# Optimization experiments

Measured on AMD Instinct MI355X. Metric: run time of the kernel, lower is better.

## Reference

```python
import jax, jax.numpy as jnp
import numpy as np

# GATConv hyperparams hardcoded in InterGraphAttention: out_channels=32, heads=2
H = 2
C = 32
N_H = 50000
N_T = 50000
E = 1600000
D = 128
NEG_SLOPE = 0.2


def setup_inputs() -> dict:
    key = jax.random.key(0)
    ks = jax.random.split(key, 9)
    h_x = jax.random.normal(ks[0], (N_H, D), dtype=jnp.float32)
    t_x = jax.random.normal(ks[1], (N_T, D), dtype=jnp.float32)
    src = jax.random.randint(ks[2], (E,), 0, N_H)
    dst = jax.random.randint(ks[3], (E,), 0, N_T)
    # PyG's add_self_loops path first removes existing self-loops; generate edges without any
    dst = jnp.where(dst == src, (dst + 1) % N_T, dst)
    edge_index = jnp.stack([src, dst]).astype(jnp.int64)
    glorot = 1.0 / np.sqrt(D)
    W_src = jax.random.normal(ks[4], (D, H * C), dtype=jnp.float32) * glorot
    W_dst = jax.random.normal(ks[5], (D, H * C), dtype=jnp.float32) * glorot
    att_src = jax.random.normal(ks[6], (H, C), dtype=jnp.float32) * (1.0 / np.sqrt(C))
    att_dst = jax.random.normal(ks[7], (H, C), dtype=jnp.float32) * (1.0 / np.sqrt(C))
    bias = jnp.zeros((H * C,), dtype=jnp.float32)
    return {"h_x": h_x, "t_x": t_x, "edge_index": edge_index,
            "W_src": W_src, "W_dst": W_dst,
            "att_src": att_src, "att_dst": att_dst, "bias": bias}


def _gat(x_src, x_dst, src, dst, W_s, W_d, a_src, a_dst, bias):
    Ns, Nd = x_src.shape[0], x_dst.shape[0]
    xs = (x_src @ W_s).reshape(Ns, H, C)   # [Ns,H,C]
    xd = (x_dst @ W_d).reshape(Nd, H, C)   # [Nd,H,C]
    al_s = jnp.einsum('nhc,hc->nh', xs, a_src)  # [Ns,H]
    al_d = jnp.einsum('nhc,hc->nh', xd, a_dst)  # [Nd,H]
    # PyG GATConv default add_self_loops=True: append i->i for i < min(Ns,Nd)
    loop = jnp.arange(min(Ns, Nd), dtype=src.dtype)
    src2 = jnp.concatenate([src, loop])
    dst2 = jnp.concatenate([dst, loop])
    alpha = jax.nn.leaky_relu(al_s[src2] + al_d[dst2], NEG_SLOPE)  # [E2,H]
    # edge-softmax over destination neighborhoods (PyG softmax: +1e-16 in denom)
    m = jax.ops.segment_max(alpha, dst2, num_segments=Nd)
    e = jnp.exp(alpha - m[dst2])
    s = jax.ops.segment_sum(e, dst2, num_segments=Nd)
    w = e / (s[dst2] + 1e-16)                                      # [E2,H]
    msg = w[:, :, None] * xs[src2]                                 # [E2,H,C]
    out = jax.ops.segment_sum(msg, dst2, num_segments=Nd)          # [Nd,H,C]
    return out.reshape(Nd, H * C) + bias


def reference(h_x, t_x, edge_index, W_src, W_dst, att_src, att_dst, bias):
    h_in = jax.nn.elu(h_x)
    t_in = jax.nn.elu(t_x)
    src, dst = edge_index[0], edge_index[1]
    t_rep = _gat(h_in, t_in, src, dst, W_src, W_dst, att_src, att_dst, bias)
    h_rep = _gat(t_in, h_in, dst, src, W_src, W_dst, att_src, att_dst, bias)
    return (h_rep, t_rep)
```

## Files before the change

### kernel.cpp

```cpp
#include <hip/hip_runtime.h>
#include <hip/hip_bf16.h>
#include <math.h>

#define HC 64
#define DD 128
#define BSH 7
#define BW  128
#define KMAX 512
#define CHUNK 4096
#define CAP 8192
#define CAPB 6144

typedef __attribute__((ext_vector_type(8))) short bf16x8;
typedef __attribute__((ext_vector_type(4))) float f32x4;

__device__ __forceinline__ unsigned short f2bf(float f) {
  unsigned u = __float_as_uint(f);
  return (unsigned short)((u + 0x7fffu + ((u >> 16) & 1u)) >> 16);
}

__global__ __launch_bounds__(128) void build_bt(
    const float* __restrict__ Wsrc, const float* __restrict__ Wdst,
    const float* __restrict__ att_src, const float* __restrict__ att_dst,
    unsigned short* __restrict__ Bt, int* __restrict__ gcur, int KK)
{
  int j = blockIdx.x;
  int k = threadIdx.x;
  const float LOG2E = 1.44269504f;
  float v = 0.f;
  if (j < 64) {
    v = Wsrc[k * HC + j];
  } else if (j < 68) {
    int hh = j - 64;
    const float* W = (hh < 2) ? Wsrc : Wdst;
    const float* a = (hh < 2) ? att_src : att_dst;
    int h = hh & 1;
    float s = 0.f;
    for (int c = 0; c < 32; ++c)
      s = fmaf(W[k * HC + h * 32 + c], a[h * 32 + c], s);
    v = s * LOG2E;
  }
  Bt[j * DD + k] = f2bf(v);
  if (j == 0) {
    for (int i = k; i < KK; i += 128) gcur[i] = 0;
  }
}

__global__ __launch_bounds__(512) void fused_front(
    const float* __restrict__ xH, const float* __restrict__ xT,
    const unsigned short* __restrict__ Bt,
    __hip_bfloat16* __restrict__ xsH, __hip_bfloat16* __restrict__ xsT,
    float* __restrict__ lsH, float* __restrict__ ldH,
    float* __restrict__ lsT, float* __restrict__ ldT,
    int NH, int NT, int blocksH, int nodeB,
    const int* __restrict__ src, const int* __restrict__ dst, int E, int NL,
    int* __restrict__ gcurA, int* __restrict__ gcurB,
    unsigned int* __restrict__ partA, unsigned int* __restrict__ partB,
    int KA, int KB)
{
  __shared__ unsigned int raw[CHUNK];
  __shared__ unsigned int stage[CHUNK];
  __shared__ int lcnt[KMAX];
  __shared__ int lbase[KMAX];
  __shared__ int lcur[KMAX];
  __shared__ int gbase[KMAX];

  int tid = threadIdx.x;

  if ((int)blockIdx.x < nodeB) {
    const float* x; __hip_bfloat16* xs; float* logit_s; float* logit_d; int N, blk;
    if ((int)blockIdx.x < blocksH) { x = xH; xs = xsH; logit_s = lsH; logit_d = ldH; N = NH; blk = blockIdx.x; }
    else { x = xT; xs = xsT; logit_s = lsT; logit_d = ldT; N = NT; blk = blockIdx.x - blocksH; }

    int wid  = tid >> 6;
    int lane = tid & 63;
    int m    = lane & 15;
    int kg   = lane >> 4;
    int nbase = (blk * 8 + wid) * 16;
    if (nbase >= N) return;
    int nrow = nbase + m;
    int nclamp = (nrow < N) ? nrow : (N - 1);

    bf16x8 ahi[4], alo[4];
    const float* xrow = x + (size_t)nclamp * DD + kg * 8;
    #pragma unroll
    for (int kt = 0; kt < 4; ++kt) {
      float4 v0 = *(const float4*)(xrow + kt * 32);
      float4 v1 = *(const float4*)(xrow + kt * 32 + 4);
      float vv[8] = {v0.x, v0.y, v0.z, v0.w, v1.x, v1.y, v1.z, v1.w};
      #pragma unroll
      for (int i = 0; i < 8; ++i) {
        float v = vv[i];
        v = (v > 0.f) ? v : (exp2f(v * 1.44269504f) - 1.f);
        unsigned hb = __float_as_uint(v) & 0xffff0000u;
        ahi[kt][i] = (short)(hb >> 16);
        alo[kt][i] = (short)f2bf(v - __uint_as_float(hb));
      }
    }

    f32x4 acc[5];
    #pragma unroll
    for (int ct = 0; ct < 5; ++ct) acc[ct] = (f32x4){0.f, 0.f, 0.f, 0.f};
    const unsigned short* bbase = Bt + m * DD + kg * 8;
    #pragma unroll
    for (int ct = 0; ct < 5; ++ct) {
      #pragma unroll
      for (int kt = 0; kt < 4; ++kt) {
        bf16x8 b = *(const bf16x8*)(bbase + ct * 16 * DD + kt * 32);
        acc[ct] = __builtin_amdgcn_mfma_f32_16x16x32_bf16(ahi[kt], b, acc[ct], 0, 0, 0);
        acc[ct] = __builtin_amdgcn_mfma_f32_16x16x32_bf16(alo[kt], b, acc[ct], 0, 0, 0);
      }
    }

    int r0 = kg * 4;
    unsigned short* xsu = (unsigned short*)xs;
    #pragma unroll
    for (int ct = 0; ct < 4; ++ct) {
      #pragma unroll
      for (int r = 0; r < 4; ++r) {
        int n = nbase + r0 + r;
        if (n < N) xsu[(size_t)n * HC + ct * 16 + m] = f2bf(acc[ct][r]);
      }
    }
    if (m < 4) {
      float* dstp = (m < 2) ? logit_s : logit_d;
      int h = m & 1;
      #pragma unroll
      for (int r = 0; r < 4; ++r) {
        int n = nbase + r0 + r;
        if (n < N) dstp[n * 2 + h] = acc[4][r];
      }
    }
    return;
  }

  int bid = blockIdx.x - nodeB;
  int base = bid * CHUNK;
  int E2 = E + NL;
  int lim = base + CHUNK < E2 ? base + CHUNK : E2;
  int cnt = lim - base;

  for (int i = base + tid; i < lim; i += 512) {
    unsigned s, d;
    if (i < E) { s = (unsigned)src[i]; d = (unsigned)dst[i]; }
    else       { s = d = (unsigned)(i - E); }
    raw[i - base] = s | (d << 16);
  }
  __syncthreads();

  for (int p = 0; p < 2; ++p) {
    const int K = p ? KB : KA;
    int* gcur = p ? gcurB : gcurA;
    unsigned int* outp = p ? partB : partA;

    for (int k2 = tid; k2 < K; k2 += 512) lcnt[k2] = 0;
    __syncthreads();
    for (int i = tid; i < cnt; i += 512) {
      unsigned w = raw[i];
      unsigned key = p ? (w & 0xffffu) : (w >> 16);
      atomicAdd(&lcnt[key >> BSH], 1);
    }
    __syncthreads();
    if (tid < 64) {
      int carry = 0;
      for (int c0 = 0; c0 < K; c0 += 64) {
        int c = c0 + tid;
        int v = (c < K) ? lcnt[c] : 0;
        int inc = v;
        #pragma unroll
        for (int o = 1; o < 64; o <<= 1) {
          int u = __shfl_up(inc, o, 64);
          if (tid >= o) inc += u;
        }
        if (c < K) lbase[c] = inc - v + carry;
        carry += __shfl(inc, 63, 64);
      }
    }
    __syncthreads();
    for (int k2 = tid; k2 < K; k2 += 512) {
      lcur[k2] = lbase[k2];
      gbase[k2] = atomicAdd(&gcur[k2], lcnt[k2]);
    }
    __syncthreads();
    for (int i = tid; i < cnt; i += 512) {
      unsigned w = raw[i];
      unsigned key = p ? (w & 0xffffu) : (w >> 16);
      unsigned val = p ? (w >> 16) : (w & 0xffffu);
      int pos = atomicAdd(&lcur[key >> BSH], 1);
      stage[pos] = val | (key << 16);
    }
    __syncthreads();
    for (int i = tid; i < cnt; i += 512) {
      unsigned wv = stage[i];
      int kk = wv >> (16 + BSH);
      outp[(size_t)kk * CAPB + gbase[kk] + (i - lbase[kk])] = wv;
    }
    __syncthreads();
  }
}

__global__ __launch_bounds__(256) void bucket_csr4(
    const unsigned int* __restrict__ partA, const int* __restrict__ cntA,
    int KA, int NA,
    const unsigned int* __restrict__ partB, const int* __restrict__ cntB,
    int KB, int NB,
    int E2, int* __restrict__ csrA, int* __restrict__ rowA,
    int* __restrict__ csrB, int* __restrict__ rowB)
{
  __shared__ int sbuf[CAP];
  __shared__ int hist[BW + 1];
  __shared__ int cur[BW];
  __shared__ int red[256];
  const unsigned int* part; const int* cntp;
  int* csr; int* row; int k, K, N;
  if ((int)blockIdx.x < KA) { k = blockIdx.x; part = partA; cntp = cntA; csr = csrA; row = rowA; K = KA; N = NA; }
  else { k = blockIdx.x - KA; part = partB; cntp = cntB; csr = csrB; row = rowB; K = KB; N = NB; }
  int tid = threadIdx.x;

  int psum = 0;
  for (int j = tid; j < k; j += 256) psum += cntp[j];
  red[tid] = psum; __syncthreads();
  for (int s = 128; s > 0; s >>= 1) {
    if (tid < s) red[tid] += red[tid + s];
    __syncthreads();
  }
  int beg = red[0];
  int cnt = cntp[k];
  size_t kbase = (size_t)k * CAPB;
  int d0 = k << BSH;
  int width = (BW < N - d0) ? BW : (N - d0);

  for (int i = tid; i <= BW; i += 256) hist[i] = 0;
  __syncthreads();
  for (int i = tid; i < cnt; i += 256)
    atomicAdd(&hist[(part[kbase + i] >> 16) & (BW - 1)], 1);
  __syncthreads();
  if (tid == 0) {
    int run = 0;
    for (int j = 0; j < width; ++j) { int c = hist[j]; hist[j] = run; run += c; }
    hist[width] = run;
  }
  __syncthreads();
  if (tid < width) { cur[tid] = hist[tid]; row[d0 + tid] = beg + hist[tid]; }
  if (k == K - 1 && tid == 0) row[N] = E2;
  __syncthreads();
  if (cnt <= CAP) {
    for (int i = tid; i < cnt; i += 256) {
      unsigned int wv = part[kbase + i];
      int pos = atomicAdd(&cur[(wv >> 16) & (BW - 1)], 1);
      sbuf[pos] = wv & 0xFFFF;
    }
    __syncthreads();
    for (int i = tid; i < cnt; i += 256) csr[beg + i] = sbuf[i];
  } else {
    for (int i = tid; i < cnt; i += 256) {
      unsigned int wv = part[kbase + i];
      int pos = atomicAdd(&cur[(wv >> 16) & (BW - 1)], 1);
      csr[beg + pos] = wv & 0xFFFF;
    }
  }
}

__device__ __forceinline__ float lrelu_clamp(float a) {
  a = (a > 0.f) ? a : 0.2f * a;
  return fminf(a, 43.f);
}

__global__ __launch_bounds__(256) void csr_message5(
    const int* __restrict__ rowA, const int* __restrict__ csrA,
    const float* __restrict__ lsA, const float* __restrict__ ldA,
    const __hip_bfloat16* __restrict__ xsA, float* __restrict__ outA, int NdA,
    const int* __restrict__ rowB, const int* __restrict__ csrB,
    const float* __restrict__ lsB, const float* __restrict__ ldB,
    const __hip_bfloat16* __restrict__ xsB, float* __restrict__ outB, int NdB,
    const float* __restrict__ bias, int blocksA)
{
  const int* row; const int* csr_src; const float* logit_s; const float* logit_d;
  const __hip_bfloat16* xs; float* out; int Nd, blk;
  if ((int)blockIdx.x < blocksA) { row = rowA; csr_src = csrA; logit_s = lsA; logit_d = ldA; xs = xsA; out = outA; Nd = NdA; blk = blockIdx.x; }
  else { row = rowB; csr_src = csrB; logit_s = lsB; logit_d = ldB; xs = xsB; out = outB; Nd = NdB; blk = blockIdx.x - blocksA; }

  __shared__ int lds[4 * 232];
  int tid  = threadIdx.x;
  int wid  = tid >> 6;
  int lane = tid & 63;
  int l31  = lane & 31;
  int half = lane >> 5;
  int head = l31 >> 4;

  int* L = &lds[wid * 232];
  float* Lf = (float*)L;
  int sv_w = (half ? 40 : 0) + l31;
  int w0_w = (half ? 160 : 80) + l31;
  int w1_w = (half ? 200 : 120) + l31;
  const int4*   svq = (const int4*)  (L  + (half ? 40 : 0));
  const float4* wq  = (const float4*)(Lf + (half ? (head ? 200 : 160)
                                                 : (head ? 120 : 80)));
  const unsigned* xs2 = (const unsigned*)xs;
  const float2* ls2 = (const float2*)logit_s;

  int d = blk * 8 + (wid << 1) + half;
  int beg = 0, end = 0;
  float2 ld2 = {0.f, 0.f};
  if (d < Nd) {
    beg = row[d]; end = row[d + 1];
    ld2 = ((const float2*)logit_d)[d];
  }

  int nt = ((end - beg) + 31) >> 5;
  nt = max(nt, __shfl_xor(nt, 32, 64));

  float2 accA = {0.f, 0.f}, accB = {0.f, 0.f};
  float s0 = 0.f, s1 = 0.f;
  int myPos = beg;

#define STEP(SV, W, ACC) {                                         \
    unsigned xv = xs2[(SV) * 32 + l31];                            \
    ACC.x = fmaf((W), __uint_as_float(xv << 16), ACC.x);           \
    ACC.y = fmaf((W), __uint_as_float(xv & 0xffff0000u), ACC.y);   \
  }

  for (int tile = 0; tile < nt; ++tile, myPos += 32) {
    int tc = end - myPos; tc = tc < 0 ? 0 : (tc > 32 ? 32 : tc);
    int sv = 0; float e0 = 0.f, e1 = 0.f;
    if (l31 < tc) {
      sv = csr_src[myPos + l31];
      float2 l2 = ls2[sv];
      e0 = exp2f(lrelu_clamp(l2.x + ld2.x));
      e1 = exp2f(lrelu_clamp(l2.y + ld2.y));
    }
    s0 += e0; s1 += e1;
    L[sv_w]       = sv;
    Lf[w0_w]      = e0;
    Lf[w1_w]      = e1;
    asm volatile("s_waitcnt lgkmcnt(0)" ::: "memory");
    int tcmax = max(tc, __shfl_xor(tc, 32, 64));
    int nq = (tcmax + 3) >> 2;
    for (int q = 0; q < nq; ++q) {
      int4   s4 = svq[q];
      float4 w4 = wq[q];
      STEP(s4.x, w4.x, accA)
      STEP(s4.y, w4.y, accB)
      STEP(s4.z, w4.z, accA)
      STEP(s4.w, w4.w, accB)
    }
  }
#undef STEP

  #pragma unroll
  for (int off = 16; off > 0; off >>= 1) {
    s0 += __shfl_xor(s0, off, 64);
    s1 += __shfl_xor(s1, off, 64);
  }
  float sD = (l31 & 16) ? s1 : s0;
  float inv = 1.f / (sD + 1e-16f);

  if (d < Nd) {
    float2 b2 = ((const float2*)bias)[l31];
    float2 o;
    o.x = (accA.x + accB.x) * inv + b2.x;
    o.y = (accA.y + accB.y) * inv + b2.y;
    ((float2*)out)[(size_t)d * 32 + l31] = o;
  }
}

extern "C" void kernel_launch(void* const* d_in, const int* in_sizes, int n_in,
                              void* d_out, int out_size, void* d_ws, size_t ws_size,
                              hipStream_t stream)
{
  const float* h_x   = (const float*)d_in[0];
  const float* t_x   = (const float*)d_in[1];
  const int*   edge  = (const int*)d_in[2];
  const float* W_src = (const float*)d_in[3];
  const float* W_dst = (const float*)d_in[4];
  const float* att_s = (const float*)d_in[5];
  const float* att_d = (const float*)d_in[6];
  const float* bias  = (const float*)d_in[7];

  int NH = in_sizes[0] / DD;
  int NT = in_sizes[1] / DD;
  int E  = in_sizes[2] / 2;
  int NL = (NH < NT) ? NH : NT;
  int E2 = E + NL;
  const int* srcA = edge;
  const int* dstA = edge + E;

  int KA = (NT + BW - 1) >> BSH;
  int KB = (NH + BW - 1) >> BSH;
  int B  = (E2 + CHUNK - 1) / CHUNK;

  char* w = (char*)d_ws;
  size_t used = 0;
  auto alloc = [&](size_t bytes) {
    char* p = w + used; used = (used + bytes + 255) & ~(size_t)255; return p;
  };
  __hip_bfloat16* xsA = (__hip_bfloat16*)alloc((size_t)NH * HC * 2);
  __hip_bfloat16* xsB = (__hip_bfloat16*)alloc((size_t)NT * HC * 2);
  float* lsA  = (float*)alloc((size_t)NH * 2 * 4);
  float* ldB  = (float*)alloc((size_t)NH * 2 * 4);
  float* lsB  = (float*)alloc((size_t)NT * 2 * 4);
  float* ldA  = (float*)alloc((size_t)NT * 2 * 4);
  int* gcur   = (int*)alloc((size_t)(KA + KB) * 4);
  int* gcurA  = gcur;
  int* gcurB  = gcur + KA;
  int* rowT   = (int*)alloc((size_t)(NT + 1) * 4);
  int* rowH   = (int*)alloc((size_t)(NH + 1) * 4);
  unsigned int* partA = (unsigned int*)alloc((size_t)KA * CAPB * 4);
  unsigned int* partB = (unsigned int*)alloc((size_t)KB * CAPB * 4);
  int* csrT   = (int*)alloc((size_t)E2 * 4);
  int* csrH   = (int*)alloc((size_t)E2 * 4);
  unsigned short* Bt = (unsigned short*)alloc((size_t)80 * DD * 2);

  float* out   = (float*)d_out;
  float* out_h = out;
  float* out_t = out + (size_t)NH * HC;

  build_bt<<<80, 128, 0, stream>>>(W_src, W_dst, att_s, att_d, Bt,
                                   gcur, KA + KB);

  int bH = (NH + 127) / 128, bT = (NT + 127) / 128;
  int nodeB = bH + bT;
  fused_front<<<nodeB + B, 512, 0, stream>>>(
      h_x, t_x, Bt, xsA, xsB, lsA, ldB, lsB, ldA, NH, NT, bH, nodeB,
      srcA, dstA, E, NL, gcurA, gcurB, partA, partB, KA, KB);

  bucket_csr4<<<KA + KB, 256, 0, stream>>>(
      partA, gcurA, KA, NT, partB, gcurB, KB, NH,
      E2, csrT, rowT, csrH, rowH);

  int gA = (NT + 7) / 8, gB = (NH + 7) / 8;
  csr_message5<<<gA + gB, 256, 0, stream>>>(
      rowT, csrT, lsA, ldA, xsA, out_t, NT,
      rowH, csrH, lsB, ldB, xsB, out_h, NH, bias, gA);
}
```

Before: 221.3 us.

## Fuse all stages into one persistent cooperative kernel with grid syncs

Replaces the four separate launches (weight prep, projection plus edge partitioning, bucket-to-CSR, message aggregation) with a single persistent cooperative kernel. Stages are separated by grid.sync, and each block loops over tiles, chunks, buckets and node groups. The goal is to remove launch gaps and inter-kernel drain and fill. In exchange, the grid size is capped by occupancy, weight prep runs on a single block, LDS use grows to the union of all stages, and message blocks change shape from 256 to 512 threads. The old multi-kernel path is kept as a fallback when cooperative launch is unavailable.

```diff
diff --git a/kernel.cpp b/kernel.cpp
--- a/kernel.cpp
+++ b/kernel.cpp
@@ -1,6 +1,9 @@
 #include <hip/hip_runtime.h>
 #include <hip/hip_bf16.h>
+#include <hip/hip_cooperative_groups.h>
 #include <math.h>
+
+namespace cg = cooperative_groups;
 
 #define HC 64
 #define DD 128
@@ -17,6 +20,329 @@
 __device__ __forceinline__ unsigned short f2bf(float f) {
   unsigned u = __float_as_uint(f);
   return (unsigned short)((u + 0x7fffu + ((u >> 16) & 1u)) >> 16);
+}
+
+__device__ __forceinline__ float lrelu_clamp(float a) {
+  a = (a > 0.f) ? a : 0.2f * a;
+  return fminf(a, 43.f);
+}
+
+struct MegaArgs {
+  const float* h_x; const float* t_x;
+  const float* Wsrc; const float* Wdst;
+  const float* att_src; const float* att_dst;
+  const float* bias;
+  const int* src; const int* dst;
+  unsigned short* Bt;
+  __hip_bfloat16* xsA; __hip_bfloat16* xsB;
+  float* lsA; float* ldB; float* lsB; float* ldA;
+  int* gcurA; int* gcurB;
+  int* rowT; int* rowH;
+  unsigned* partA; unsigned* partB;
+  int* csrT; int* csrH;
+  float* out_h; float* out_t;
+  int NH, NT, E, NL, KA, KB;
+};
+
+union SMem {
+  struct { unsigned raw[CHUNK]; unsigned stage[CHUNK];
+           int lcnt[KMAX]; int lbase[KMAX]; int lcur[KMAX]; int gbase[KMAX]; } part;
+  struct { int sbuf[CAP]; int hist[BW + 1]; int cur[BW]; int red[512]; } bkt;
+  struct { int lds[8 * 232]; } msg;
+};
+
+__global__ __launch_bounds__(512) void mega(MegaArgs a)
+{
+  cg::grid_group grid = cg::this_grid();
+  __shared__ SMem sm;
+  const int tid = threadIdx.x;
+  const int E2 = a.E + a.NL;
+  const int tilesH = (a.NH + 127) >> 7, tilesT = (a.NT + 127) >> 7;
+  const int ntiles = tilesH + tilesT;
+  const int nchunks = (E2 + CHUNK - 1) / CHUNK;
+  const float LOG2E = 1.44269504f;
+
+  if (blockIdx.x == 0) {
+    for (int i = tid; i < 80 * DD; i += 512) {
+      int j = i >> 7, k = i & 127;
+      float v = 0.f;
+      if (j < 64) {
+        v = a.Wsrc[k * HC + j];
+      } else if (j < 68) {
+        int hh = j - 64;
+        const float* W = (hh < 2) ? a.Wsrc : a.Wdst;
+        const float* at = (hh < 2) ? a.att_src : a.att_dst;
+        int h = hh & 1;
+        float s = 0.f;
+        for (int c = 0; c < 32; ++c)
+          s = fmaf(W[k * HC + h * 32 + c], at[h * 32 + c], s);
+        v = s * LOG2E;
+      }
+      a.Bt[j * DD + k] = f2bf(v);
+    }
+  } else if (blockIdx.x == 1) {
+    for (int i = tid; i < a.KA + a.KB; i += 512) a.gcurA[i] = 0;
+  }
+  __threadfence();
+  grid.sync();
+
+  for (int it = blockIdx.x; it < ntiles + nchunks; it += gridDim.x) {
+    if (it < ntiles) {
+      const float* x; __hip_bfloat16* xs; float* logit_s; float* logit_d; int N, blk;
+      if (it < tilesH) { x = a.h_x; xs = a.xsA; logit_s = a.lsA; logit_d = a.ldB; N = a.NH; blk = it; }
+      else { x = a.t_x; xs = a.xsB; logit_s = a.lsB; logit_d = a.ldA; N = a.NT; blk = it - tilesH; }
+      int wid = tid >> 6, lane = tid & 63, m = lane & 15, kg = lane >> 4;
+      int nbase = (blk * 8 + wid) * 16;
+      if (nbase < N) {
+        int nrow = nbase + m;
+        int nclamp = (nrow < N) ? nrow : (N - 1);
+        bf16x8 ahi[4], alo[4];
+        const float* xrow = x + (size_t)nclamp * DD + kg * 8;
+        #pragma unroll
+        for (int kt = 0; kt < 4; ++kt) {
+          float4 v0 = *(const float4*)(xrow + kt * 32);
+          float4 v1 = *(const float4*)(xrow + kt * 32 + 4);
+          float vv[8] = {v0.x, v0.y, v0.z, v0.w, v1.x, v1.y, v1.z, v1.w};
+          #pragma unroll
+          for (int i = 0; i < 8; ++i) {
+            float v = vv[i];
+            v = (v > 0.f) ? v : (exp2f(v * 1.44269504f) - 1.f);
+            unsigned hb = __float_as_uint(v) & 0xffff0000u;
+            ahi[kt][i] = (short)(hb >> 16);
+            alo[kt][i] = (short)f2bf(v - __uint_as_float(hb));
+          }
+        }
+        f32x4 acc[5];
+        #pragma unroll
+        for (int ct = 0; ct < 5; ++ct) acc[ct] = (f32x4){0.f, 0.f, 0.f, 0.f};
+        const unsigned short* bbase = a.Bt + m * DD + kg * 8;
+        #pragma unroll
+        for (int ct = 0; ct < 5; ++ct) {
+          #pragma unroll
+          for (int kt = 0; kt < 4; ++kt) {
+            bf16x8 b = *(const bf16x8*)(bbase + ct * 16 * DD + kt * 32);
+            acc[ct] = __builtin_amdgcn_mfma_f32_16x16x32_bf16(ahi[kt], b, acc[ct], 0, 0, 0);
+            acc[ct] = __builtin_amdgcn_mfma_f32_16x16x32_bf16(alo[kt], b, acc[ct], 0, 0, 0);
+          }
+        }
+        int r0 = kg * 4;
+        unsigned short* xsu = (unsigned short*)xs;
+        #pragma unroll
+        for (int ct = 0; ct < 4; ++ct) {
+          #pragma unroll
+          for (int r = 0; r < 4; ++r) {
+            int n = nbase + r0 + r;
+            if (n < N) xsu[(size_t)n * HC + ct * 16 + m] = f2bf(acc[ct][r]);
+          }
+        }
+        if (m < 4) {
+          float* dstp = (m < 2) ? logit_s : logit_d;
+          int h = m & 1;
+          #pragma unroll
+          for (int r = 0; r < 4; ++r) {
+            int n = nbase + r0 + r;
+            if (n < N) dstp[n * 2 + h] = acc[4][r];
+          }
+        }
+      }
+    } else {
+      int bid = it - ntiles;
+      int base = bid * CHUNK;
+      int lim = base + CHUNK < E2 ? base + CHUNK : E2;
+      int cnt = lim - base;
+      for (int i = base + tid; i < lim; i += 512) {
+        unsigned s, d;
+        if (i < a.E) { s = (unsigned)a.src[i]; d = (unsigned)a.dst[i]; }
+        else         { s = d = (unsigned)(i - a.E); }
+        sm.part.raw[i - base] = s | (d << 16);
+      }
+      __syncthreads();
+      for (int p = 0; p < 2; ++p) {
+        const int K = p ? a.KB : a.KA;
+        int* gcur = p ? a.gcurB : a.gcurA;
+        unsigned* outp = p ? a.partB : a.partA;
+        for (int k2 = tid; k2 < K; k2 += 512) sm.part.lcnt[k2] = 0;
+        __syncthreads();
+        for (int i = tid; i < cnt; i += 512) {
+          unsigned w = sm.part.raw[i];
+          unsigned key = p ? (w & 0xffffu) : (w >> 16);
+          atomicAdd(&sm.part.lcnt[key >> BSH], 1);
+        }
+        __syncthreads();
+        if (tid < 64) {
+          int carry = 0;
+          for (int c0 = 0; c0 < K; c0 += 64) {
+            int c = c0 + tid;
+            int v = (c < K) ? sm.part.lcnt[c] : 0;
+            int inc = v;
+            #pragma unroll
+            for (int o = 1; o < 64; o <<= 1) {
+              int u = __shfl_up(inc, o, 64);
+              if (tid >= o) inc += u;
+            }
+            if (c < K) sm.part.lbase[c] = inc - v + carry;
+            carry += __shfl(inc, 63, 64);
+          }
+        }
+        __syncthreads();
+        for (int k2 = tid; k2 < K; k2 += 512) {
+          sm.part.lcur[k2] = sm.part.lbase[k2];
+          sm.part.gbase[k2] = atomicAdd(&gcur[k2], sm.part.lcnt[k2]);
+        }
+        __syncthreads();
+        for (int i = tid; i < cnt; i += 512) {
+          unsigned w = sm.part.raw[i];
+          unsigned key = p ? (w & 0xffffu) : (w >> 16);
+          unsigned val = p ? (w >> 16) : (w & 0xffffu);
+          int pos = atomicAdd(&sm.part.lcur[key >> BSH], 1);
+          sm.part.stage[pos] = val | (key << 16);
+        }
+        __syncthreads();
+        for (int i = tid; i < cnt; i += 512) {
+          unsigned wv = sm.part.stage[i];
+          int kk = wv >> (16 + BSH);
+          outp[(size_t)kk * CAPB + sm.part.gbase[kk] + (i - sm.part.lbase[kk])] = wv;
+        }
+        __syncthreads();
+      }
+    }
+  }
+  __threadfence();
+  grid.sync();
+
+  for (int bb = blockIdx.x; bb < a.KA + a.KB; bb += gridDim.x) {
+    const unsigned* part; const int* cntp; int* csr; int* row; int k, K, N;
+    if (bb < a.KA) { k = bb; part = a.partA; cntp = a.gcurA; csr = a.csrT; row = a.rowT; K = a.KA; N = a.NT; }
+    else { k = bb - a.KA; part = a.partB; cntp = a.gcurB; csr = a.csrH; row = a.rowH; K = a.KB; N = a.NH; }
+
+    int psum = 0;
+    for (int j = tid; j < k; j += 512) psum += cntp[j];
+    sm.bkt.red[tid] = psum; __syncthreads();
+    for (int s = 256; s > 0; s >>= 1) {
+      if (tid < s) sm.bkt.red[tid] += sm.bkt.red[tid + s];
+      __syncthreads();
+    }
+    int beg = sm.bkt.red[0];
+    int cnt = cntp[k];
+    size_t kbase = (size_t)k * CAPB;
+    int d0 = k << BSH;
+    int width = (BW < N - d0) ? BW : (N - d0);
+
+    for (int i = tid; i <= BW; i += 512) sm.bkt.hist[i] = 0;
+    __syncthreads();
+    for (int i = tid; i < cnt; i += 512)
+      atomicAdd(&sm.bkt.hist[(part[kbase + i] >> 16) & (BW - 1)], 1);
+    __syncthreads();
+    if (tid == 0) {
+      int run = 0;
+      for (int j = 0; j < width; ++j) { int c = sm.bkt.hist[j]; sm.bkt.hist[j] = run; run += c; }
+      sm.bkt.hist[width] = run;
+    }
+    __syncthreads();
+    if (tid < width) { sm.bkt.cur[tid] = sm.bkt.hist[tid]; row[d0 + tid] = beg + sm.bkt.hist[tid]; }
+    if (k == K - 1 && tid == 0) row[N] = E2;
+    __syncthreads();
+    if (cnt <= CAP) {
+      for (int i = tid; i < cnt; i += 512) {
+        unsigned wv = part[kbase + i];
+        int pos = atomicAdd(&sm.bkt.cur[(wv >> 16) & (BW - 1)], 1);
+        sm.bkt.sbuf[pos] = wv & 0xFFFF;
+      }
+      __syncthreads();
+      for (int i = tid; i < cnt; i += 512) csr[beg + i] = sm.bkt.sbuf[i];
+    } else {
+      for (int i = tid; i < cnt; i += 512) {
+        unsigned wv = part[kbase + i];
+        int pos = atomicAdd(&sm.bkt.cur[(wv >> 16) & (BW - 1)], 1);
+        csr[beg + pos] = wv & 0xFFFF;
+      }
+    }
+    __syncthreads();
+  }
+  __threadfence();
+  grid.sync();
+
+  {
+    int wid = tid >> 6, lane = tid & 63, l31 = lane & 31, half = lane >> 5;
+    int head = l31 >> 4;
+    int* L = sm.msg.lds + wid * 232;
+    float* Lf = (float*)L;
+    int sv_w = (half ? 40 : 0) + l31;
+    int w0_w = (half ? 160 : 80) + l31;
+    int w1_w = (half ? 200 : 120) + l31;
+    const int4*   svq = (const int4*)  (L  + (half ? 40 : 0));
+    const float4* wq  = (const float4*)(Lf + (half ? (head ? 200 : 160)
+                                                   : (head ? 120 : 80)));
+    int ngA = (a.NT + 15) >> 4, ngB = (a.NH + 15) >> 4;
+    for (int g = blockIdx.x; g < ngA + ngB; g += gridDim.x) {
+      const int* row; const int* csr_src; const float* logit_s; const float* logit_d;
+      const __hip_bfloat16* xs; float* out; int Nd, gblk;
+      if (g < ngA) { row = a.rowT; csr_src = a.csrT; logit_s = a.lsA; logit_d = a.ldA; xs = a.xsA; out = a.out_t; Nd = a.NT; gblk = g; }
+      else { row = a.rowH; csr_src = a.csrH; logit_s = a.lsB; logit_d = a.ldB; xs = a.xsB; out = a.out_h; Nd = a.NH; gblk = g - ngA; }
+      const unsigned* xs2 = (const unsigned*)xs;
+      const float2* ls2 = (const float2*)logit_s;
+
+      int d = gblk * 16 + (wid << 1) + half;
+      int beg = 0, end = 0;
+      float2 ld2 = {0.f, 0.f};
+      if (d < Nd) {
+        beg = row[d]; end = row[d + 1];
+        ld2 = ((const float2*)logit_d)[d];
+      }
+      int nt = ((end - beg) + 31) >> 5;
+      nt = max(nt, __shfl_xor(nt, 32, 64));
+
+      float2 accA = {0.f, 0.f}, accB = {0.f, 0.f};
+      float s0 = 0.f, s1 = 0.f;
+      int myPos = beg;
+
+#define STEP(SV, W, ACC) {                                         \
+      unsigned xv = xs2[(SV) * 32 + l31];                          \
+      ACC.x = fmaf((W), __uint_as_float(xv << 16), ACC.x);         \
+      ACC.y = fmaf((W), __uint_as_float(xv & 0xffff0000u), ACC.y); \
+    }
+      for (int tile = 0; tile < nt; ++tile, myPos += 32) {
+        int tc = end - myPos; tc = tc < 0 ? 0 : (tc > 32 ? 32 : tc);
+        int sv = 0; float e0 = 0.f, e1 = 0.f;
+        if (l31 < tc) {
+          sv = csr_src[myPos + l31];
+          float2 l2 = ls2[sv];
+          e0 = exp2f(lrelu_clamp(l2.x + ld2.x));
+          e1 = exp2f(lrelu_clamp(l2.y + ld2.y));
+        }
+        s0 += e0; s1 += e1;
+        L[sv_w]  = sv;
+        Lf[w0_w] = e0;
+        Lf[w1_w] = e1;
+        asm volatile("s_waitcnt lgkmcnt(0)" ::: "memory");
+        int tcmax = max(tc, __shfl_xor(tc, 32, 64));
+        int nq = (tcmax + 3) >> 2;
+        for (int q = 0; q < nq; ++q) {
+          int4   s4 = svq[q];
+          float4 w4 = wq[q];
+          STEP(s4.x, w4.x, accA)
+          STEP(s4.y, w4.y, accB)
+          STEP(s4.z, w4.z, accA)
+          STEP(s4.w, w4.w, accB)
+        }
+      }
+#undef STEP
+      #pragma unroll
+      for (int off = 16; off > 0; off >>= 1) {
+        s0 += __shfl_xor(s0, off, 64);
+        s1 += __shfl_xor(s1, off, 64);
+      }
+      float sD = (l31 & 16) ? s1 : s0;
+      float inv = 1.f / (sD + 1e-16f);
+      if (d < Nd) {
+        float2 b2 = ((const float2*)a.bias)[l31];
+        float2 o;
+        o.x = (accA.x + accB.x) * inv + b2.x;
+        o.y = (accA.y + accB.y) * inv + b2.y;
+        ((float2*)out)[(size_t)d * 32 + l31] = o;
+      }
+    }
+  }
 }
 
 __global__ __launch_bounds__(128) void build_bt(
@@ -64,14 +390,12 @@
   __shared__ int lbase[KMAX];
   __shared__ int lcur[KMAX];
   __shared__ int gbase[KMAX];
-
   int tid = threadIdx.x;
 
   if ((int)blockIdx.x < nodeB) {
     const float* x; __hip_bfloat16* xs; float* logit_s; float* logit_d; int N, blk;
     if ((int)blockIdx.x < blocksH) { x = xH; xs = xsH; logit_s = lsH; logit_d = ldH; N = NH; blk = blockIdx.x; }
     else { x = xT; xs = xsT; logit_s = lsT; logit_d = ldT; N = NT; blk = blockIdx.x - blocksH; }
-
     int wid  = tid >> 6;
     int lane = tid & 63;
     int m    = lane & 15;
@@ -80,7 +404,6 @@
     if (nbase >= N) return;
     int nrow = nbase + m;
     int nclamp = (nrow < N) ? nrow : (N - 1);
-
     bf16x8 ahi[4], alo[4];
     const float* xrow = x + (size_t)nclamp * DD + kg * 8;
     #pragma unroll
@@ -97,7 +420,6 @@
         alo[kt][i] = (short)f2bf(v - __uint_as_float(hb));
       }
     }
-
     f32x4 acc[5];
     #pragma unroll
     for (int ct = 0; ct < 5; ++ct) acc[ct] = (f32x4){0.f, 0.f, 0.f, 0.f};
@@ -111,7 +433,6 @@
         acc[ct] = __builtin_amdgcn_mfma_f32_16x16x32_bf16(alo[kt], b, acc[ct], 0, 0, 0);
       }
     }
-
     int r0 = kg * 4;
     unsigned short* xsu = (unsigned short*)xs;
     #pragma unroll
@@ -139,7 +460,6 @@
   int E2 = E + NL;
   int lim = base + CHUNK < E2 ? base + CHUNK : E2;
   int cnt = lim - base;
-
   for (int i = base + tid; i < lim; i += 512) {
     unsigned s, d;
     if (i < E) { s = (unsigned)src[i]; d = (unsigned)dst[i]; }
@@ -147,12 +467,10 @@
     raw[i - base] = s | (d << 16);
   }
   __syncthreads();
-
   for (int p = 0; p < 2; ++p) {
     const int K = p ? KB : KA;
     int* gcur = p ? gcurB : gcurA;
     unsigned int* outp = p ? partB : partA;
-
     for (int k2 = tid; k2 < K; k2 += 512) lcnt[k2] = 0;
     __syncthreads();
     for (int i = tid; i < cnt; i += 512) {
@@ -216,7 +534,6 @@
   if ((int)blockIdx.x < KA) { k = blockIdx.x; part = partA; cntp = cntA; csr = csrA; row = rowA; K = KA; N = NA; }
   else { k = blockIdx.x - KA; part = partB; cntp = cntB; csr = csrB; row = rowB; K = KB; N = NB; }
   int tid = threadIdx.x;
-
   int psum = 0;
   for (int j = tid; j < k; j += 256) psum += cntp[j];
   red[tid] = psum; __syncthreads();
@@ -229,7 +546,6 @@
   size_t kbase = (size_t)k * CAPB;
   int d0 = k << BSH;
   int width = (BW < N - d0) ? BW : (N - d0);
-
   for (int i = tid; i <= BW; i += 256) hist[i] = 0;
   __syncthreads();
   for (int i = tid; i < cnt; i += 256)
@@ -259,11 +575,6 @@
       csr[beg + pos] = wv & 0xFFFF;
     }
   }
-}
-
-__device__ __forceinline__ float lrelu_clamp(float a) {
-  a = (a > 0.f) ? a : 0.2f * a;
-  return fminf(a, 43.f);
 }
 
 __global__ __launch_bounds__(256) void csr_message5(
@@ -279,7 +590,6 @@
   const __hip_bfloat16* xs; float* out; int Nd, blk;
   if ((int)blockIdx.x < blocksA) { row = rowA; csr_src = csrA; logit_s = lsA; logit_d = ldA; xs = xsA; out = outA; Nd = NdA; blk = blockIdx.x; }
   else { row = rowB; csr_src = csrB; logit_s = lsB; logit_d = ldB; xs = xsB; out = outB; Nd = NdB; blk = blockIdx.x - blocksA; }
-
   __shared__ int lds[4 * 232];
   int tid  = threadIdx.x;
   int wid  = tid >> 6;
@@ -287,7 +597,6 @@
   int l31  = lane & 31;
   int half = lane >> 5;
   int head = l31 >> 4;
-
   int* L = &lds[wid * 232];
   float* Lf = (float*)L;
   int sv_w = (half ? 40 : 0) + l31;
@@ -298,7 +607,6 @@
                                                  : (head ? 120 : 80)));
   const unsigned* xs2 = (const unsigned*)xs;
   const float2* ls2 = (const float2*)logit_s;
-
   int d = blk * 8 + (wid << 1) + half;
   int beg = 0, end = 0;
   float2 ld2 = {0.f, 0.f};
@@ -306,20 +614,16 @@
     beg = row[d]; end = row[d + 1];
     ld2 = ((const float2*)logit_d)[d];
   }
-
   int nt = ((end - beg) + 31) >> 5;
   nt = max(nt, __shfl_xor(nt, 32, 64));
-
   float2 accA = {0.f, 0.f}, accB = {0.f, 0.f};
   float s0 = 0.f, s1 = 0.f;
   int myPos = beg;
-
 #define STEP(SV, W, ACC) {                                         \
     unsigned xv = xs2[(SV) * 32 + l31];                            \
     ACC.x = fmaf((W), __uint_as_float(xv << 16), ACC.x);           \
     ACC.y = fmaf((W), __uint_as_float(xv & 0xffff0000u), ACC.y);   \
   }
-
   for (int tile = 0; tile < nt; ++tile, myPos += 32) {
     int tc = end - myPos; tc = tc < 0 ? 0 : (tc > 32 ? 32 : tc);
     int sv = 0; float e0 = 0.f, e1 = 0.f;
@@ -330,9 +634,9 @@
       e1 = exp2f(lrelu_clamp(l2.y + ld2.y));
     }
     s0 += e0; s1 += e1;
-    L[sv_w]       = sv;
-    Lf[w0_w]      = e0;
-    Lf[w1_w]      = e1;
+    L[sv_w]  = sv;
+    Lf[w0_w] = e0;
+    Lf[w1_w] = e1;
     asm volatile("s_waitcnt lgkmcnt(0)" ::: "memory");
     int tcmax = max(tc, __shfl_xor(tc, 32, 64));
     int nq = (tcmax + 3) >> 2;
@@ -346,7 +650,6 @@
     }
   }
 #undef STEP
-
   #pragma unroll
   for (int off = 16; off > 0; off >>= 1) {
     s0 += __shfl_xor(s0, off, 64);
@@ -354,7 +657,6 @@
   }
   float sD = (l31 & 16) ? s1 : s0;
   float inv = 1.f / (sD + 1e-16f);
-
   if (d < Nd) {
     float2 b2 = ((const float2*)bias)[l31];
     float2 o;
@@ -415,19 +717,52 @@
   float* out_h = out;
   float* out_t = out + (size_t)NH * HC;
 
+  static int coop = -1;
+  static int gridSize = 0;
+  if (coop < 0) {
+    int dev = 0; hipGetDevice(&dev);
+    int ca = 0;
+    hipDeviceGetAttribute(&ca, hipDeviceAttributeCooperativeLaunch, dev);
+    int nCU = 0;
+    hipDeviceGetAttribute(&nCU, hipDeviceAttributeMultiprocessorCount, dev);
+    int nbpc = 0;
+    hipError_t e = hipOccupancyMaxActiveBlocksPerMultiprocessor(
+        &nbpc, (const void*)mega, 512, 0);
+    if (e != hipSuccess || nbpc < 1 || nCU < 1) ca = 0;
+    gridSize = nCU * nbpc;
+    coop = ca ? 1 : 0;
+  }
+
+  if (coop && gridSize > 1) {
+    MegaArgs ma;
+    ma.h_x = h_x; ma.t_x = t_x; ma.Wsrc = W_src; ma.Wdst = W_dst;
+    ma.att_src = att_s; ma.att_dst = att_d; ma.bias = bias;
+    ma.src = srcA; ma.dst = dstA; ma.Bt = Bt;
+    ma.xsA = xsA; ma.xsB = xsB;
+    ma.lsA = lsA; ma.ldB = ldB; ma.lsB = lsB; ma.ldA = ldA;
+    ma.gcurA = gcurA; ma.gcurB = gcurB;
+    ma.rowT = rowT; ma.rowH = rowH;
+    ma.partA = partA; ma.partB = partB;
+    ma.csrT = csrT; ma.csrH = csrH;
+    ma.out_h = out_h; ma.out_t = out_t;
+    ma.NH = NH; ma.NT = NT; ma.E = E; ma.NL = NL; ma.KA = KA; ma.KB = KB;
+    void* args[] = { &ma };
+    hipError_t err = hipLaunchCooperativeKernel(
+        (const void*)mega, dim3(gridSize), dim3(512), args, 0, stream);
+    if (err == hipSuccess) return;
+    coop = 0;
+  }
+
   build_bt<<<80, 128, 0, stream>>>(W_src, W_dst, att_s, att_d, Bt,
                                    gcur, KA + KB);
-
   int bH = (NH + 127) / 128, bT = (NT + 127) / 128;
   int nodeB = bH + bT;
   fused_front<<<nodeB + B, 512, 0, stream>>>(
       h_x, t_x, Bt, xsA, xsB, lsA, ldB, lsB, ldA, NH, NT, bH, nodeB,
       srcA, dstA, E, NL, gcurA, gcurB, partA, partB, KA, KB);
-
   bucket_csr4<<<KA + KB, 256, 0, stream>>>(
       partA, gcurA, KA, NT, partB, gcurB, KB, NH,
       E2, csrT, rowT, csrH, rowH);
-
   int gA = (NT + 7) / 8, gB = (NH + 7) / 8;
   csr_message5<<<gA + gB, 256, 0, stream>>>(
       rowT, csrT, lsA, ldA, xsA, out_t, NT,
```

Result: slower. 566.9 us (+156.2%).

## Fuse bucket CSR build with message aggregation into one kernel

Applied to the files above, without the earlier changes.

Merges the per-bucket counting sort and the per-destination softmax/aggregation into a single kernel. Each 512-thread block sorts its bucket's edges into shared memory and then processes its 128 destinations directly from that buffer. This removes the global CSR and row arrays, the prefix-sum reduction, and one kernel launch. The cost is much coarser parallelism: only about 782 blocks each process 128 destinations serially over 8 passes. Overflow buckets fall back to a slow full scan of the bucket for every destination.

```diff
diff --git a/kernel.cpp b/kernel.cpp
--- a/kernel.cpp
+++ b/kernel.cpp
@@ -17,6 +17,11 @@
 __device__ __forceinline__ unsigned short f2bf(float f) {
   unsigned u = __float_as_uint(f);
   return (unsigned short)((u + 0x7fffu + ((u >> 16) & 1u)) >> 16);
+}
+
+__device__ __forceinline__ float lrelu_clamp(float a) {
+  a = (a > 0.f) ? a : 0.2f * a;
+  return fminf(a, 43.f);
 }
 
 __global__ __launch_bounds__(128) void build_bt(
@@ -64,14 +69,12 @@
   __shared__ int lbase[KMAX];
   __shared__ int lcur[KMAX];
   __shared__ int gbase[KMAX];
-
   int tid = threadIdx.x;
 
   if ((int)blockIdx.x < nodeB) {
     const float* x; __hip_bfloat16* xs; float* logit_s; float* logit_d; int N, blk;
     if ((int)blockIdx.x < blocksH) { x = xH; xs = xsH; logit_s = lsH; logit_d = ldH; N = NH; blk = blockIdx.x; }
     else { x = xT; xs = xsT; logit_s = lsT; logit_d = ldT; N = NT; blk = blockIdx.x - blocksH; }
-
     int wid  = tid >> 6;
     int lane = tid & 63;
     int m    = lane & 15;
@@ -80,7 +83,6 @@
     if (nbase >= N) return;
     int nrow = nbase + m;
     int nclamp = (nrow < N) ? nrow : (N - 1);
-
     bf16x8 ahi[4], alo[4];
     const float* xrow = x + (size_t)nclamp * DD + kg * 8;
     #pragma unroll
@@ -97,7 +99,6 @@
         alo[kt][i] = (short)f2bf(v - __uint_as_float(hb));
       }
     }
-
     f32x4 acc[5];
     #pragma unroll
     for (int ct = 0; ct < 5; ++ct) acc[ct] = (f32x4){0.f, 0.f, 0.f, 0.f};
@@ -111,7 +112,6 @@
         acc[ct] = __builtin_amdgcn_mfma_f32_16x16x32_bf16(alo[kt], b, acc[ct], 0, 0, 0);
       }
     }
-
     int r0 = kg * 4;
     unsigned short* xsu = (unsigned short*)xs;
     #pragma unroll
@@ -139,7 +139,6 @@
   int E2 = E + NL;
   int lim = base + CHUNK < E2 ? base + CHUNK : E2;
   int cnt = lim - base;
-
   for (int i = base + tid; i < lim; i += 512) {
     unsigned s, d;
     if (i < E) { s = (unsigned)src[i]; d = (unsigned)dst[i]; }
@@ -147,12 +146,10 @@
     raw[i - base] = s | (d << 16);
   }
   __syncthreads();
-
   for (int p = 0; p < 2; ++p) {
     const int K = p ? KB : KA;
     int* gcur = p ? gcurB : gcurA;
     unsigned int* outp = p ? partB : partA;
-
     for (int k2 = tid; k2 < K; k2 += 512) lcnt[k2] = 0;
     __syncthreads();
     for (int i = tid; i < cnt; i += 512) {
@@ -199,40 +196,39 @@
   }
 }
 
-__global__ __launch_bounds__(256) void bucket_csr4(
-    const unsigned int* __restrict__ partA, const int* __restrict__ cntA,
-    int KA, int NA,
-    const unsigned int* __restrict__ partB, const int* __restrict__ cntB,
-    int KB, int NB,
-    int E2, int* __restrict__ csrA, int* __restrict__ rowA,
-    int* __restrict__ csrB, int* __restrict__ rowB)
+__global__ __launch_bounds__(512) void bucket_message(
+    const unsigned* __restrict__ partA, const int* __restrict__ cntA, int KA, int NA,
+    const unsigned* __restrict__ partB, const int* __restrict__ cntB, int KB, int NB,
+    const float* __restrict__ lsA, const float* __restrict__ ldA,
+    const __hip_bfloat16* __restrict__ xsA, float* __restrict__ outA,
+    const float* __restrict__ lsB, const float* __restrict__ ldB,
+    const __hip_bfloat16* __restrict__ xsB, float* __restrict__ outB,
+    const float* __restrict__ bias)
 {
   __shared__ int sbuf[CAP];
   __shared__ int hist[BW + 1];
   __shared__ int cur[BW];
-  __shared__ int red[256];
-  const unsigned int* part; const int* cntp;
-  int* csr; int* row; int k, K, N;
-  if ((int)blockIdx.x < KA) { k = blockIdx.x; part = partA; cntp = cntA; csr = csrA; row = rowA; K = KA; N = NA; }
-  else { k = blockIdx.x - KA; part = partB; cntp = cntB; csr = csrB; row = rowB; K = KB; N = NB; }
+  __shared__ int mlds[8 * 232];
+
+  const unsigned* part; const int* cntp; int k, N;
+  const float* logit_s; const float* logit_d; const __hip_bfloat16* xs; float* out;
+  if ((int)blockIdx.x < KA) {
+    k = blockIdx.x; part = partA; cntp = cntA; N = NA;
+    logit_s = lsA; logit_d = ldA; xs = xsA; out = outA;
+  } else {
+    k = blockIdx.x - KA; part = partB; cntp = cntB; N = NB;
+    logit_s = lsB; logit_d = ldB; xs = xsB; out = outB;
+  }
+
   int tid = threadIdx.x;
-
-  int psum = 0;
-  for (int j = tid; j < k; j += 256) psum += cntp[j];
-  red[tid] = psum; __syncthreads();
-  for (int s = 128; s > 0; s >>= 1) {
-    if (tid < s) red[tid] += red[tid + s];
-    __syncthreads();
-  }
-  int beg = red[0];
   int cnt = cntp[k];
   size_t kbase = (size_t)k * CAPB;
   int d0 = k << BSH;
   int width = (BW < N - d0) ? BW : (N - d0);
 
-  for (int i = tid; i <= BW; i += 256) hist[i] = 0;
-  __syncthreads();
-  for (int i = tid; i < cnt; i += 256)
+  for (int i = tid; i <= BW; i += 512) hist[i] = 0;
+  __syncthreads();
+  for (int i = tid; i < cnt; i += 512)
     atomicAdd(&hist[(part[kbase + i] >> 16) & (BW - 1)], 1);
   __syncthreads();
   if (tid == 0) {
@@ -241,54 +237,24 @@
     hist[width] = run;
   }
   __syncthreads();
-  if (tid < width) { cur[tid] = hist[tid]; row[d0 + tid] = beg + hist[tid]; }
-  if (k == K - 1 && tid == 0) row[N] = E2;
-  __syncthreads();
-  if (cnt <= CAP) {
-    for (int i = tid; i < cnt; i += 256) {
-      unsigned int wv = part[kbase + i];
+  if (tid < width) cur[tid] = hist[tid];
+  __syncthreads();
+  bool fits = (cnt <= CAP);
+  if (fits) {
+    for (int i = tid; i < cnt; i += 512) {
+      unsigned wv = part[kbase + i];
       int pos = atomicAdd(&cur[(wv >> 16) & (BW - 1)], 1);
-      sbuf[pos] = wv & 0xFFFF;
-    }
-    __syncthreads();
-    for (int i = tid; i < cnt; i += 256) csr[beg + i] = sbuf[i];
-  } else {
-    for (int i = tid; i < cnt; i += 256) {
-      unsigned int wv = part[kbase + i];
-      int pos = atomicAdd(&cur[(wv >> 16) & (BW - 1)], 1);
-      csr[beg + pos] = wv & 0xFFFF;
-    }
-  }
-}
-
-__device__ __forceinline__ float lrelu_clamp(float a) {
-  a = (a > 0.f) ? a : 0.2f * a;
-  return fminf(a, 43.f);
-}
-
-__global__ __launch_bounds__(256) void csr_message5(
-    const int* __restrict__ rowA, const int* __restrict__ csrA,
-    const float* __restrict__ lsA, const float* __restrict__ ldA,
-    const __hip_bfloat16* __restrict__ xsA, float* __restrict__ outA, int NdA,
-    const int* __restrict__ rowB, const int* __restrict__ csrB,
-    const float* __restrict__ lsB, const float* __restrict__ ldB,
-    const __hip_bfloat16* __restrict__ xsB, float* __restrict__ outB, int NdB,
-    const float* __restrict__ bias, int blocksA)
-{
-  const int* row; const int* csr_src; const float* logit_s; const float* logit_d;
-  const __hip_bfloat16* xs; float* out; int Nd, blk;
-  if ((int)blockIdx.x < blocksA) { row = rowA; csr_src = csrA; logit_s = lsA; logit_d = ldA; xs = xsA; out = outA; Nd = NdA; blk = blockIdx.x; }
-  else { row = rowB; csr_src = csrB; logit_s = lsB; logit_d = ldB; xs = xsB; out = outB; Nd = NdB; blk = blockIdx.x - blocksA; }
-
-  __shared__ int lds[4 * 232];
-  int tid  = threadIdx.x;
+      sbuf[pos] = (int)(wv & 0xFFFFu);
+    }
+  }
+  __syncthreads();
+
   int wid  = tid >> 6;
   int lane = tid & 63;
   int l31  = lane & 31;
   int half = lane >> 5;
   int head = l31 >> 4;
-
-  int* L = &lds[wid * 232];
+  int* L = mlds + wid * 232;
   float* Lf = (float*)L;
   int sv_w = (half ? 40 : 0) + l31;
   int w0_w = (half ? 160 : 80) + l31;
@@ -299,69 +265,122 @@
   const unsigned* xs2 = (const unsigned*)xs;
   const float2* ls2 = (const float2*)logit_s;
 
-  int d = blk * 8 + (wid << 1) + half;
-  int beg = 0, end = 0;
-  float2 ld2 = {0.f, 0.f};
-  if (d < Nd) {
-    beg = row[d]; end = row[d + 1];
-    ld2 = ((const float2*)logit_d)[d];
-  }
-
-  int nt = ((end - beg) + 31) >> 5;
-  nt = max(nt, __shfl_xor(nt, 32, 64));
-
-  float2 accA = {0.f, 0.f}, accB = {0.f, 0.f};
-  float s0 = 0.f, s1 = 0.f;
-  int myPos = beg;
-
 #define STEP(SV, W, ACC) {                                         \
     unsigned xv = xs2[(SV) * 32 + l31];                            \
     ACC.x = fmaf((W), __uint_as_float(xv << 16), ACC.x);           \
     ACC.y = fmaf((W), __uint_as_float(xv & 0xffff0000u), ACC.y);   \
   }
 
-  for (int tile = 0; tile < nt; ++tile, myPos += 32) {
-    int tc = end - myPos; tc = tc < 0 ? 0 : (tc > 32 ? 32 : tc);
-    int sv = 0; float e0 = 0.f, e1 = 0.f;
-    if (l31 < tc) {
-      sv = csr_src[myPos + l31];
-      float2 l2 = ls2[sv];
-      e0 = exp2f(lrelu_clamp(l2.x + ld2.x));
-      e1 = exp2f(lrelu_clamp(l2.y + ld2.y));
-    }
-    s0 += e0; s1 += e1;
-    L[sv_w]       = sv;
-    Lf[w0_w]      = e0;
-    Lf[w1_w]      = e1;
-    asm volatile("s_waitcnt lgkmcnt(0)" ::: "memory");
-    int tcmax = max(tc, __shfl_xor(tc, 32, 64));
-    int nq = (tcmax + 3) >> 2;
-    for (int q = 0; q < nq; ++q) {
-      int4   s4 = svq[q];
-      float4 w4 = wq[q];
-      STEP(s4.x, w4.x, accA)
-      STEP(s4.y, w4.y, accB)
-      STEP(s4.z, w4.z, accA)
-      STEP(s4.w, w4.w, accB)
+  if (fits) {
+    for (int p = 0; p < 8; ++p) {
+      int dl = p * 16 + (wid << 1) + half;
+      int d = d0 + dl;
+      int beg = 0, end = 0;
+      float2 ld2 = {0.f, 0.f};
+      if (dl < width) {
+        beg = hist[dl]; end = hist[dl + 1];
+        ld2 = ((const float2*)logit_d)[d];
+      }
+      int nt = ((end - beg) + 31) >> 5;
+      nt = max(nt, __shfl_xor(nt, 32, 64));
+
+      float2 accA = {0.f, 0.f}, accB = {0.f, 0.f};
+      float s0 = 0.f, s1 = 0.f;
+      int myPos = beg;
+      for (int tile = 0; tile < nt; ++tile, myPos += 32) {
+        int tc = end - myPos; tc = tc < 0 ? 0 : (tc > 32 ? 32 : tc);
+        int sv = 0; float e0 = 0.f, e1 = 0.f;
+        if (l31 < tc) {
+          sv = sbuf[myPos + l31];
+          float2 l2 = ls2[sv];
+          e0 = exp2f(lrelu_clamp(l2.x + ld2.x));
+          e1 = exp2f(lrelu_clamp(l2.y + ld2.y));
+        }
+        s0 += e0; s1 += e1;
+        L[sv_w]  = sv;
+        Lf[w0_w] = e0;
+        Lf[w1_w] = e1;
+        asm volatile("s_waitcnt lgkmcnt(0)" ::: "memory");
+        int tcmax = max(tc, __shfl_xor(tc, 32, 64));
+        int nq = (tcmax + 3) >> 2;
+        for (int q = 0; q < nq; ++q) {
+          int4   s4 = svq[q];
+          float4 w4 = wq[q];
+          STEP(s4.x, w4.x, accA)
+          STEP(s4.y, w4.y, accB)
+          STEP(s4.z, w4.z, accA)
+          STEP(s4.w, w4.w, accB)
+        }
+      }
+      #pragma unroll
+      for (int off = 16; off > 0; off >>= 1) {
+        s0 += __shfl_xor(s0, off, 64);
+        s1 += __shfl_xor(s1, off, 64);
+      }
+      float sD = (l31 & 16) ? s1 : s0;
+      float inv = 1.f / (sD + 1e-16f);
+      if (dl < width) {
+        float2 b2 = ((const float2*)bias)[l31];
+        float2 o;
+        o.x = (accA.x + accB.x) * inv + b2.x;
+        o.y = (accA.y + accB.y) * inv + b2.y;
+        ((float2*)out)[(size_t)d * 32 + l31] = o;
+      }
+    }
+  } else {
+    for (int p = 0; p < 8; ++p) {
+      int dl = p * 16 + (wid << 1) + half;
+      int d = d0 + dl;
+      bool act = (dl < width);
+      float2 ld2 = {0.f, 0.f};
+      if (act) ld2 = ((const float2*)logit_d)[d];
+      float2 accA = {0.f, 0.f}, accB = {0.f, 0.f};
+      float s0 = 0.f, s1 = 0.f;
+      for (int t0 = 0; t0 < cnt; t0 += 32) {
+        int idx = t0 + l31;
+        int sv = 0; float e0 = 0.f, e1 = 0.f;
+        if (idx < cnt) {
+          unsigned wv = part[kbase + idx];
+          sv = (int)(wv & 0xFFFFu);
+          if (act && (int)((wv >> 16) & (BW - 1)) == dl) {
+            float2 l2 = ls2[sv];
+            e0 = exp2f(lrelu_clamp(l2.x + ld2.x));
+            e1 = exp2f(lrelu_clamp(l2.y + ld2.y));
+          }
+        }
+        s0 += e0; s1 += e1;
+        L[sv_w]  = sv;
+        Lf[w0_w] = e0;
+        Lf[w1_w] = e1;
+        asm volatile("s_waitcnt lgkmcnt(0)" ::: "memory");
+        int rem = cnt - t0; int tcmax = rem < 32 ? rem : 32;
+        int nq = (tcmax + 3) >> 2;
+        for (int q = 0; q < nq; ++q) {
+          int4   s4 = svq[q];
+          float4 w4 = wq[q];
+          STEP(s4.x, w4.x, accA)
+          STEP(s4.y, w4.y, accB)
+          STEP(s4.z, w4.z, accA)
+          STEP(s4.w, w4.w, accB)
+        }
+      }
+      #pragma unroll
+      for (int off = 16; off > 0; off >>= 1) {
+        s0 += __shfl_xor(s0, off, 64);
+        s1 += __shfl_xor(s1, off, 64);
+      }
+      float sD = (l31 & 16) ? s1 : s0;
+      float inv = 1.f / (sD + 1e-16f);
+      if (act) {
+        float2 b2 = ((const float2*)bias)[l31];
+        float2 o;
+        o.x = (accA.x + accB.x) * inv + b2.x;
+        o.y = (accA.y + accB.y) * inv + b2.y;
+        ((float2*)out)[(size_t)d * 32 + l31] = o;
+      }
     }
   }
 #undef STEP
-
-  #pragma unroll
-  for (int off = 16; off > 0; off >>= 1) {
-    s0 += __shfl_xor(s0, off, 64);
-    s1 += __shfl_xor(s1, off, 64);
-  }
-  float sD = (l31 & 16) ? s1 : s0;
-  float inv = 1.f / (sD + 1e-16f);
-
-  if (d < Nd) {
-    float2 b2 = ((const float2*)bias)[l31];
-    float2 o;
-    o.x = (accA.x + accB.x) * inv + b2.x;
-    o.y = (accA.y + accB.y) * inv + b2.y;
-    ((float2*)out)[(size_t)d * 32 + l31] = o;
-  }
 }
 
 extern "C" void kernel_launch(void* const* d_in, const int* in_sizes, int n_in,
@@ -403,12 +422,8 @@
   int* gcur   = (int*)alloc((size_t)(KA + KB) * 4);
   int* gcurA  = gcur;
   int* gcurB  = gcur + KA;
-  int* rowT   = (int*)alloc((size_t)(NT + 1) * 4);
-  int* rowH   = (int*)alloc((size_t)(NH + 1) * 4);
   unsigned int* partA = (unsigned int*)alloc((size_t)KA * CAPB * 4);
   unsigned int* partB = (unsigned int*)alloc((size_t)KB * CAPB * 4);
-  int* csrT   = (int*)alloc((size_t)E2 * 4);
-  int* csrH   = (int*)alloc((size_t)E2 * 4);
   unsigned short* Bt = (unsigned short*)alloc((size_t)80 * DD * 2);
 
   float* out   = (float*)d_out;
@@ -424,12 +439,8 @@
       h_x, t_x, Bt, xsA, xsB, lsA, ldB, lsB, ldA, NH, NT, bH, nodeB,
       srcA, dstA, E, NL, gcurA, gcurB, partA, partB, KA, KB);
 
-  bucket_csr4<<<KA + KB, 256, 0, stream>>>(
+  bucket_message<<<KA + KB, 512, 0, stream>>>(
       partA, gcurA, KA, NT, partB, gcurB, KB, NH,
-      E2, csrT, rowT, csrH, rowH);
-
-  int gA = (NT + 7) / 8, gB = (NH + 7) / 8;
-  csr_message5<<<gA + gB, 256, 0, stream>>>(
-      rowT, csrT, lsA, ldA, xsA, out_t, NT,
-      rowH, csrH, lsB, ldB, xsB, out_h, NH, bias, gA);
-}
+      lsA, ldA, xsA, out_t,
+      lsB, ldB, xsB, out_h, bias);
+}
```

Measured after the change: 263.4 us. +19.0%, slower.
